# Kernel tuning notes

Hardware: AMD Instinct MI355X
Metric: run time of the kernel (lower is better)

## Reference

```python
import jax, jax.numpy as jnp
import numpy as np

A_THRESH = 0.5  # module-level `a`
P_THRESH = 0.5  # module-level `p`
B, IN, H = 131072, 3, 256
D = IN + H


def setup_inputs() -> dict:
    key = jax.random.key(0)
    ks = jax.random.split(key, 7)
    lim = 1.0 / np.sqrt(D)  # torch nn.Linear default uniform(-1/sqrt(fan_in), ...)
    return {
        "input_tensor": jax.random.normal(ks[0], (B, IN), dtype=jnp.float32),
        "h_cur": jax.random.normal(ks[1], (B, H), dtype=jnp.float32),
        "c_cur": jax.random.normal(ks[2], (B, H), dtype=jnp.float32),
        # fused [i|f|g|o] gate weights, stored [in, out]
        "W_gates": jax.random.uniform(ks[3], (D, 4 * H), minval=-lim, maxval=lim, dtype=jnp.float32),
        "b_gates": jax.random.uniform(ks[4], (4 * H,), minval=-lim, maxval=lim, dtype=jnp.float32),
        # switch gates init.normal_(std=0.01), fused [w_i|w_g]
        "W_switch": 0.01 * jax.random.normal(ks[5], (D, 2), dtype=jnp.float32),
        "b_switch": 0.01 * jax.random.normal(ks[6], (2,), dtype=jnp.float32),
    }


def reference(input_tensor, h_cur, c_cur, W_gates, b_gates, W_switch, b_switch):
    combined = jnp.concatenate([input_tensor, h_cur], axis=1)  # [B, D]
    gates = combined @ W_gates + b_gates                       # [B, 4H]
    h = h_cur.shape[1]
    i = jax.nn.sigmoid(gates[:, :h])
    f = jax.nn.sigmoid(gates[:, h:2 * h])
    g = jnp.tanh(gates[:, 2 * h:3 * h])
    o = jax.nn.sigmoid(gates[:, 3 * h:])

    sw = jax.nn.sigmoid(combined @ W_switch + b_switch)        # [B, 2]
    w_i, w_g = sw[:, 0], sw[:, 1]

    n = w_g.shape[0]
    thr = n * A_THRESH
    cnt_g = jnp.sum(w_g > P_THRESH)
    cnt_i = jnp.sum(w_i > P_THRESH)

    fc = f * c_cur
    c_next_i = fc + i
    c_next_g = fc + g
    c_next_ig = fc + i * g

    cond_i = (cnt_g < thr) & (cnt_i > thr)
    cond_g = (cnt_g > thr) & (cnt_i < thr)
    c_next = jnp.where(cond_i, c_next_i, jnp.where(cond_g, c_next_g, c_next_ig))
    h_next = o * jnp.tanh(c_next)
    return h_next, c_next
```

## Files before the change

kernel.cpp:

```cpp
#include <hip/hip_runtime.h>

#define BROWS 131072

typedef __attribute__((ext_vector_type(8))) __bf16 bf16x8;
typedef __attribute__((ext_vector_type(4))) __bf16 bf16x4;
typedef __attribute__((ext_vector_type(4))) float f32x4;

__device__ __forceinline__ float sigmoidf_(float x) {
    return 1.0f / (1.0f + __expf(-x));
}
__device__ __forceinline__ float tanhf_(float x) {
    return 1.0f - 2.0f / (__expf(2.0f * x) + 1.0f);
}

__global__ __launch_bounds__(256)
void wt_kernel(const float* __restrict__ Wg, __bf16* __restrict__ WT) {
    int gid = blockIdx.x * 256 + threadIdx.x;
    int c = gid >> 5;
    int k8 = (gid & 31) * 8;
    bf16x8 v;
#pragma unroll
    for (int j = 0; j < 8; ++j)
        v[j] = (__bf16)Wg[(3 + k8 + j) * 1024 + c];
    *(bf16x8*)(WT + c * 256 + k8) = v;
}

__global__ __launch_bounds__(256)
void switch_kernel(const float* __restrict__ x, const float* __restrict__ h,
                   const float* __restrict__ Wsw, const float* __restrict__ bsw,
                   int* __restrict__ cnt) {
    __shared__ float hs[256 * 33];
    __shared__ float wpk[512];
    const int tid = threadIdx.x;
    const int r0 = blockIdx.x * 256;

    *(float2*)&wpk[2 * tid] = *(const float2*)&Wsw[(3 + tid) * 2];

    const int row = r0 + tid;
    const float x0 = x[row * 3 + 0];
    const float x1 = x[row * 3 + 1];
    const float x2 = x[row * 3 + 2];
    float si = x0 * Wsw[0] + x1 * Wsw[2] + x2 * Wsw[4] + bsw[0];
    float sg = x0 * Wsw[1] + x1 * Wsw[3] + x2 * Wsw[5] + bsw[1];

    for (int kc = 0; kc < 8; ++kc) {
        __syncthreads();
#pragma unroll
        for (int i = 0; i < 8; ++i) {
            int idx = tid + 256 * i;
            int r = idx >> 3;
            int c4 = (idx & 7) * 4;
            float4 v = *(const float4*)(h + (r0 + r) * 256 + kc * 32 + c4);
            hs[r * 33 + c4 + 0] = v.x;
            hs[r * 33 + c4 + 1] = v.y;
            hs[r * 33 + c4 + 2] = v.z;
            hs[r * 33 + c4 + 3] = v.w;
        }
        __syncthreads();
#pragma unroll
        for (int c2 = 0; c2 < 16; ++c2) {
            float4 wv = *(const float4*)&wpk[kc * 64 + c2 * 4];
            float v0 = hs[tid * 33 + c2 * 2 + 0];
            float v1 = hs[tid * 33 + c2 * 2 + 1];
            si += v0 * wv.x + v1 * wv.z;
            sg += v0 * wv.y + v1 * wv.w;
        }
    }

    unsigned long long bi = __ballot(si > 0.0f);
    unsigned long long bgm = __ballot(sg > 0.0f);
    if ((tid & 63) == 0) {
        atomicAdd(&cnt[0], (int)__popcll(bi));
        atomicAdd(&cnt[1], (int)__popcll(bgm));
    }
}

__global__ __launch_bounds__(256)
void lstm_main(const float* __restrict__ x,
               const float* __restrict__ h,
               const float* __restrict__ c_cur,
               const float* __restrict__ Wg,
               const float* __restrict__ bg,
               const __bf16* __restrict__ WT,
               const int* __restrict__ cnt,
               float* __restrict__ out) {
    __shared__ __bf16 A_lds[128 * 40];

    const int tid = threadIdx.x;
    const int lane = tid & 63;
    const int w = tid >> 6;
    const int q = lane >> 4;
    const int ln = lane & 15;

    const int bid = blockIdx.x;
    const int jseq = bid >> 3;
    const int m0 = (((bid & 7) << 7) + (jseq >> 3)) << 7;
    const int j0 = (jseq & 7) << 5;

    const int wrow = (w >> 1) * 64;
    const int colh = j0 + (w & 1) * 16 + ln;

    const int ci = cnt[0], cg = cnt[1];
    const bool cond_i = (cg < 65536) && (ci > 65536);
    const bool cond_g = (cg > 65536) && (ci < 65536);

    f32x4 acc[4][4];
    float bcol[4], wx0[4], wx1[4], wx2[4];
#pragma unroll
    for (int nt = 0; nt < 4; ++nt) {
        int colg = nt * 256 + colh;
        bcol[nt] = bg[colg];
        wx0[nt] = Wg[0 * 1024 + colg];
        wx1[nt] = Wg[1 * 1024 + colg];
        wx2[nt] = Wg[2 * 1024 + colg];
    }
#pragma unroll
    for (int mt = 0; mt < 4; ++mt) {
#pragma unroll
        for (int r = 0; r < 4; ++r) {
            int row = m0 + wrow + mt * 16 + q * 4 + r;
            float x0 = x[row * 3 + 0];
            float x1 = x[row * 3 + 1];
            float x2 = x[row * 3 + 2];
#pragma unroll
            for (int nt = 0; nt < 4; ++nt) {
                acc[mt][nt][r] = bcol[nt] + x0 * wx0[nt] + x1 * wx1[nt] + x2 * wx2[nt];
            }
        }
    }

    float4 areg[4];
#pragma unroll
    for (int i = 0; i < 4; ++i) {
        int idx = tid + 256 * i;
        int row = idx >> 3, kq = idx & 7;
        areg[i] = *(const float4*)(h + (m0 + row) * 256 + 0 * 32 + kq * 4);
    }

    const __bf16* wtb[4];
#pragma unroll
    for (int nt = 0; nt < 4; ++nt)
        wtb[nt] = WT + (nt * 256 + colh) * 256 + q * 8;

    for (int kc = 0; kc < 8; ++kc) {
        if (kc) __syncthreads();
#pragma unroll
        for (int i = 0; i < 4; ++i) {
            int idx = tid + 256 * i;
            int row = idx >> 3, kq = idx & 7;
            bf16x4 v;
            v[0] = (__bf16)areg[i].x;
            v[1] = (__bf16)areg[i].y;
            v[2] = (__bf16)areg[i].z;
            v[3] = (__bf16)areg[i].w;
            *(bf16x4*)(&A_lds[row * 40 + kq * 4]) = v;
        }
        __syncthreads();
        if (kc < 7) {
#pragma unroll
            for (int i = 0; i < 4; ++i) {
                int idx = tid + 256 * i;
                int row = idx >> 3, kq = idx & 7;
                areg[i] = *(const float4*)(h + (m0 + row) * 256 + (kc + 1) * 32 + kq * 4);
            }
        }
        bf16x8 bfrag[4];
#pragma unroll
        for (int nt = 0; nt < 4; ++nt)
            bfrag[nt] = *(const bf16x8*)(wtb[nt] + kc * 32);
        bf16x8 afrag[4];
#pragma unroll
        for (int mt = 0; mt < 4; ++mt)
            afrag[mt] = *(const bf16x8*)(&A_lds[(wrow + mt * 16 + ln) * 40 + q * 8]);
#pragma unroll
        for (int mt = 0; mt < 4; ++mt)
#pragma unroll
            for (int nt = 0; nt < 4; ++nt)
                acc[mt][nt] = __builtin_amdgcn_mfma_f32_16x16x32_bf16(
                    afrag[mt], bfrag[nt], acc[mt][nt], 0, 0, 0);
    }

#pragma unroll
    for (int mt = 0; mt < 4; ++mt) {
#pragma unroll
        for (int r = 0; r < 4; ++r) {
            int row = m0 + wrow + mt * 16 + q * 4 + r;
            float gi = sigmoidf_(acc[mt][0][r]);
            float gf = sigmoidf_(acc[mt][1][r]);
            float gg = tanhf_(acc[mt][2][r]);
            float go = sigmoidf_(acc[mt][3][r]);
            float c = c_cur[row * 256 + colh];
            float X = cond_i ? gi : (cond_g ? gg : gi * gg);
            float cn = gf * c + X;
            float hn = go * tanhf_(cn);
            out[row * 256 + colh] = hn;
            out[BROWS * 256 + row * 256 + colh] = cn;
        }
    }
}

extern "C" void kernel_launch(void* const* d_in, const int* in_sizes, int n_in,
                              void* d_out, int out_size, void* d_ws, size_t ws_size,
                              hipStream_t stream) {
    const float* x   = (const float*)d_in[0];
    const float* h   = (const float*)d_in[1];
    const float* c   = (const float*)d_in[2];
    const float* Wg  = (const float*)d_in[3];
    const float* bg  = (const float*)d_in[4];
    const float* Wsw = (const float*)d_in[5];
    const float* bsw = (const float*)d_in[6];
    float* out = (float*)d_out;

    int* cnt = (int*)d_ws;
    __bf16* WT = (__bf16*)((char*)d_ws + 1024);

    hipMemsetAsync(d_ws, 0, 8, stream);
    wt_kernel<<<128, 256, 0, stream>>>(Wg, WT);
    switch_kernel<<<512, 256, 0, stream>>>(x, h, Wsw, bsw, cnt);
    lstm_main<<<8192, 256, 0, stream>>>(x, h, c, Wg, bg, WT, cnt, out);
}
```

Measured before the change: 717.0 us.

## Load A fragments directly from global memory, drop LDS staging and syncs

The main LSTM GEMM kernel no longer stages h tiles through shared memory with barriers. Each lane now reads its own MFMA A-fragment straight from global memory, converts it to bf16 in registers, and the k-loop is unrolled. The switch kernel likewise drops its LDS transpose and reads each row's h directly with float4 loads. This removes barriers and LDS traffic, but global accesses become strided per lane (each lane reads a different row) and the same h data is reloaded by both column-half waves, relying on the cache.

Result: slower. 901.4 us (+25.7%).

```diff
diff --git a/kernel.cpp b/kernel.cpp
--- a/kernel.cpp
+++ b/kernel.cpp
@@ -3,7 +3,6 @@
 #define BROWS 131072
 
 typedef __attribute__((ext_vector_type(8))) __bf16 bf16x8;
-typedef __attribute__((ext_vector_type(4))) __bf16 bf16x4;
 typedef __attribute__((ext_vector_type(4))) float f32x4;
 
 __device__ __forceinline__ float sigmoidf_(float x) {
@@ -29,49 +28,31 @@
 void switch_kernel(const float* __restrict__ x, const float* __restrict__ h,
                    const float* __restrict__ Wsw, const float* __restrict__ bsw,
                    int* __restrict__ cnt) {
-    __shared__ float hs[256 * 33];
-    __shared__ float wpk[512];
-    const int tid = threadIdx.x;
-    const int r0 = blockIdx.x * 256;
+    const int row = blockIdx.x * 256 + threadIdx.x;
+    const float* hr = h + (size_t)row * 256;
 
-    *(float2*)&wpk[2 * tid] = *(const float2*)&Wsw[(3 + tid) * 2];
-
-    const int row = r0 + tid;
     const float x0 = x[row * 3 + 0];
     const float x1 = x[row * 3 + 1];
     const float x2 = x[row * 3 + 2];
     float si = x0 * Wsw[0] + x1 * Wsw[2] + x2 * Wsw[4] + bsw[0];
     float sg = x0 * Wsw[1] + x1 * Wsw[3] + x2 * Wsw[5] + bsw[1];
 
-    for (int kc = 0; kc < 8; ++kc) {
-        __syncthreads();
-#pragma unroll
-        for (int i = 0; i < 8; ++i) {
-            int idx = tid + 256 * i;
-            int r = idx >> 3;
-            int c4 = (idx & 7) * 4;
-            float4 v = *(const float4*)(h + (r0 + r) * 256 + kc * 32 + c4);
-            hs[r * 33 + c4 + 0] = v.x;
-            hs[r * 33 + c4 + 1] = v.y;
-            hs[r * 33 + c4 + 2] = v.z;
-            hs[r * 33 + c4 + 3] = v.w;
-        }
-        __syncthreads();
-#pragma unroll
-        for (int c2 = 0; c2 < 16; ++c2) {
-            float4 wv = *(const float4*)&wpk[kc * 64 + c2 * 4];
-            float v0 = hs[tid * 33 + c2 * 2 + 0];
-            float v1 = hs[tid * 33 + c2 * 2 + 1];
-            si += v0 * wv.x + v1 * wv.z;
-            sg += v0 * wv.y + v1 * wv.w;
-        }
+#pragma unroll 8
+    for (int c4 = 0; c4 < 64; ++c4) {
+        float4 v = *(const float4*)(hr + c4 * 4);
+        float2 wa = *(const float2*)&Wsw[(3 + c4 * 4 + 0) * 2];
+        float2 wb = *(const float2*)&Wsw[(3 + c4 * 4 + 1) * 2];
+        float2 wc = *(const float2*)&Wsw[(3 + c4 * 4 + 2) * 2];
+        float2 wd = *(const float2*)&Wsw[(3 + c4 * 4 + 3) * 2];
+        si += v.x * wa.x + v.y * wb.x + v.z * wc.x + v.w * wd.x;
+        sg += v.x * wa.y + v.y * wb.y + v.z * wc.y + v.w * wd.y;
     }
 
     unsigned long long bi = __ballot(si > 0.0f);
-    unsigned long long bgm = __ballot(sg > 0.0f);
-    if ((tid & 63) == 0) {
+    unsigned long long bg = __ballot(sg > 0.0f);
+    if ((threadIdx.x & 63) == 0) {
         atomicAdd(&cnt[0], (int)__popcll(bi));
-        atomicAdd(&cnt[1], (int)__popcll(bgm));
+        atomicAdd(&cnt[1], (int)__popcll(bg));
     }
 }
 
@@ -84,8 +65,6 @@
                const __bf16* __restrict__ WT,
                const int* __restrict__ cnt,
                float* __restrict__ out) {
-    __shared__ __bf16 A_lds[128 * 40];
-
     const int tid = threadIdx.x;
     const int lane = tid & 63;
     const int w = tid >> 6;
@@ -129,49 +108,34 @@
         }
     }
 
-    float4 areg[4];
+    const float* habase[4];
 #pragma unroll
-    for (int i = 0; i < 4; ++i) {
-        int idx = tid + 256 * i;
-        int row = idx >> 3, kq = idx & 7;
-        areg[i] = *(const float4*)(h + (m0 + row) * 256 + 0 * 32 + kq * 4);
-    }
+    for (int mt = 0; mt < 4; ++mt)
+        habase[mt] = h + (size_t)(m0 + wrow + mt * 16 + ln) * 256 + q * 8;
 
     const __bf16* wtb[4];
 #pragma unroll
     for (int nt = 0; nt < 4; ++nt)
         wtb[nt] = WT + (nt * 256 + colh) * 256 + q * 8;
 
+#pragma unroll 4
     for (int kc = 0; kc < 8; ++kc) {
-        if (kc) __syncthreads();
+        bf16x8 afrag[4];
 #pragma unroll
-        for (int i = 0; i < 4; ++i) {
-            int idx = tid + 256 * i;
-            int row = idx >> 3, kq = idx & 7;
-            bf16x4 v;
-            v[0] = (__bf16)areg[i].x;
-            v[1] = (__bf16)areg[i].y;
-            v[2] = (__bf16)areg[i].z;
-            v[3] = (__bf16)areg[i].w;
-            *(bf16x4*)(&A_lds[row * 40 + kq * 4]) = v;
-        }
-        __syncthreads();
-        if (kc < 7) {
-#pragma unroll
-            for (int i = 0; i < 4; ++i) {
-                int idx = tid + 256 * i;
-                int row = idx >> 3, kq = idx & 7;
-                areg[i] = *(const float4*)(h + (m0 + row) * 256 + (kc + 1) * 32 + kq * 4);
-            }
+        for (int mt = 0; mt < 4; ++mt) {
+            float4 a0 = *(const float4*)(habase[mt] + kc * 32);
+            float4 a1 = *(const float4*)(habase[mt] + kc * 32 + 4);
+            bf16x8 v;
+            v[0] = (__bf16)a0.x; v[1] = (__bf16)a0.y;
+            v[2] = (__bf16)a0.z; v[3] = (__bf16)a0.w;
+            v[4] = (__bf16)a1.x; v[5] = (__bf16)a1.y;
+            v[6] = (__bf16)a1.z; v[7] = (__bf16)a1.w;
+            afrag[mt] = v;
         }
         bf16x8 bfrag[4];
 #pragma unroll
         for (int nt = 0; nt < 4; ++nt)
             bfrag[nt] = *(const bf16x8*)(wtb[nt] + kc * 32);
-        bf16x8 afrag[4];
-#pragma unroll
-        for (int mt = 0; mt < 4; ++mt)
-            afrag[mt] = *(const bf16x8*)(&A_lds[(wrow + mt * 16 + ln) * 40 + q * 8]);
 #pragma unroll
         for (int mt = 0; mt < 4; ++mt)
 #pragma unroll
```
